# Performance work log

Hardware: AMD Instinct MI355X
Metric: run time of the kernel (lower is better)

## Reference

```python
import jax, jax.numpy as jnp
import numpy as np

B, F, M, N, H, O = 8, 128, 256, 1024, 64, 128
BN_EPS = 1e-5
COS_EPS = 1e-8


def _bn(x, g, b, m, v):
    # inference-mode BatchNorm over channel axis 1
    shape = [1] * x.ndim
    shape[1] = -1
    return g.reshape(shape) * (x - m.reshape(shape)) * jax.lax.rsqrt(v.reshape(shape) + BN_EPS) + b.reshape(shape)


def setup_inputs() -> dict:
    key = jax.random.key(0)
    ks = jax.random.split(key, 24)
    def n(k, shape, s=1.0):
        return jax.random.normal(k, shape, dtype=jnp.float32) * s
    inp = {}
    inp['template_feature'] = n(ks[0], (B, F, M))
    inp['search_feature'] = n(ks[1], (B, F, N))
    # SharedMLP 1x1 conv weights (bias=False because bn=True)
    inp['W1'] = n(ks[2], (H, F + 1), 0.05)
    inp['W2'] = n(ks[3], (H, H), 0.05)
    inp['W3'] = n(ks[4], (H, H), 0.05)
    # fea_layer: conv1d(H, bn=True) then conv1d(O, activation=None, bias=True)
    inp['Wc1'] = n(ks[5], (H, H), 0.05)
    inp['Wc2'] = n(ks[6], (O, H), 0.05)
    inp['bc2'] = n(ks[7], (O,), 0.05)
    for i, nm in enumerate(['1', '2', '3', 'c1']):
        inp['g' + nm] = 1.0 + n(ks[8 + i], (H,), 0.1)
        inp['b' + nm] = n(ks[12 + i], (H,), 0.1)
        inp['m' + nm] = n(ks[16 + i], (H,), 0.01)
        inp['v' + nm] = jax.random.uniform(ks[20 + i], (H,), minval=0.5, maxval=1.5, dtype=jnp.float32)
    return inp


def reference(template_feature, search_feature, W1, W2, W3, Wc1, Wc2, bc2,
              g1, b1, m1, v1, g2, b2, m2, v2, g3, b3, m3, v3, gc1, bc1, mc1, vc1):
    t, s = template_feature, search_feature
    # pairwise cosine similarity over channel dim (no BxFxMxN expand needed)
    dot = jnp.einsum('bfm,bfn->bmn', t, s)
    nt = jnp.linalg.norm(t, axis=1)  # (B, M)
    ns = jnp.linalg.norm(s, axis=1)  # (B, N)
    cos = dot / jnp.maximum(nt[:, :, None] * ns[:, None, :], COS_EPS)  # (B, M, N)
    # first 1x1 conv on concat(cos, expand(t)) computed fused (no concat materialization)
    h = jnp.einsum('hf,bfm->bhm', W1[:, 1:], t)[..., None] + W1[:, 0][None, :, None, None] * cos[:, None]
    h = jax.nn.relu(_bn(h, g1, b1, m1, v1))  # (B, H, M, N)
    h = jax.nn.relu(_bn(jnp.einsum('gh,bhmn->bgmn', W2, h), g2, b2, m2, v2))
    h = jax.nn.relu(_bn(jnp.einsum('gh,bhmn->bgmn', W3, h), g3, b3, m3, v3))
    p = jnp.max(h, axis=2)  # max-pool over M -> (B, H, N)
    c = jax.nn.relu(_bn(jnp.einsum('gh,bhn->bgn', Wc1, p), gc1, bc1, mc1, vc1))
    return jnp.einsum('oh,bhn->bon', Wc2, c) + bc2[None, :, None]  # (B, O, N)
```

## Files before the change

kernel.cpp:

```cpp
#include <hip/hip_runtime.h>


#define BB 8
#define FF 128
#define MM 256
#define NN 1024
#define HH 64
#define OO 128
#define BN_EPS 1e-5f
#define COS_EPS 1e-8f

#define WS_U     0
#define WS_C2    64
#define WS_C3    128
#define WS_CC1   192
#define WS_W2F   256
#define WS_W3F   4352
#define WS_WC1F  8448
#define WS_A1    12544
#define WS_NT    143616
#define WS_NS    145664
#define WS_COSH  153856
#define WS_P     1202432
#define PS       524288

typedef _Float16 half2v __attribute__((ext_vector_type(2)));
typedef _Float16 half8  __attribute__((ext_vector_type(8)));
typedef __attribute__((ext_vector_type(4))) float f32x4;

__device__ __forceinline__ unsigned int pkh2(float a, float b){
  auto h = __builtin_amdgcn_cvt_pkrtz(a, b);
  return __builtin_bit_cast(unsigned int, h);
}
__device__ __forceinline__ half2v u2h(unsigned int u){
  return __builtin_bit_cast(half2v, u);
}
__device__ __forceinline__ unsigned int h2u(half2v v){
  return __builtin_bit_cast(unsigned int, v);
}
__device__ __forceinline__ unsigned int relu2(unsigned int d){
  half2v v = __builtin_elementwise_max(u2h(d), (half2v){(_Float16)0, (_Float16)0});
  return h2u(v);
}
__device__ __forceinline__ unsigned int bh1(unsigned int up, half2v c, unsigned int ap){
  half2v v = __builtin_elementwise_fma(u2h(up), c, u2h(ap));
  v = __builtin_elementwise_max(v, (half2v){(_Float16)0, (_Float16)0});
  return h2u(v);
}
__device__ __forceinline__ float dot4(float4 a, float4 b, float acc){
  acc = fmaf(a.x, b.x, acc); acc = fmaf(a.y, b.y, acc);
  acc = fmaf(a.z, b.z, acc); acc = fmaf(a.w, b.w, acc);
  return acc;
}

__global__ __launch_bounds__(256) void k_prep(const float* t_, const float* s_,
    const float* W1, const float* W2, const float* W3, const float* Wc1,
    const float* g1, const float* b1, const float* m1, const float* v1,
    const float* g2, const float* b2, const float* m2, const float* v2,
    const float* g3, const float* b3, const float* m3, const float* v3,
    const float* gc1,const float* bc1,const float* mc1,const float* vc1,
    float* ws){
  __shared__ float W1s[64][133];
  int t = threadIdx.x;
  int bx = blockIdx.x;
  if (bx < 256){
    int b = bx >> 5, m0 = (bx & 31)*8;
    for (int idx = t; idx < 8192; idx += 256){
      int h = idx >> 7, f = idx & 127;
      W1s[h][f] = W1[h*129 + 1 + f];
    }
    __syncthreads();
    int h = t & 63, mg = t >> 6;
    const float* tp = t_ + (size_t)b*FF*MM + m0 + mg*2;
    float acc0 = 0.f, acc1 = 0.f;
    for (int f = 0; f < FF; f++){
      float wv = W1s[h][f];
      float2 tv = *(const float2*)&tp[(size_t)f*MM];
      acc0 = fmaf(wv, tv.x, acc0); acc1 = fmaf(wv, tv.y, acc1);
    }
    float a1 = g1[h] / sqrtf(v1[h] + BN_EPS);
    float c1 = b1[h] - a1*m1[h];
    unsigned short* dst = (unsigned short*)(ws + WS_A1) + ((size_t)(b*MM + m0 + mg*2))*64 + h;
    dst[0]  = (unsigned short)(pkh2(fmaf(a1, acc0, c1), 0.f) & 0xFFFFu);
    dst[64] = (unsigned short)(pkh2(fmaf(a1, acc1, c1), 0.f) & 0xFFFFu);
  } else if (bx < 416){
    __shared__ float red[4][64];
    int x = t & 63, fq = t >> 6;
    int idx = (bx - 256)*64 + x;
    const float* ptr; size_t stride;
    if (idx < BB*MM){
      int b = idx >> 8, m = idx & 255;
      ptr = t_ + (size_t)b*FF*MM + m; stride = MM;
    } else {
      int j = idx - BB*MM;
      int b = j >> 10, n = j & 1023;
      ptr = s_ + (size_t)b*FF*NN + n; stride = NN;
    }
    float acc = 0.f;
    for (int f = fq*32; f < fq*32 + 32; f++){
      float v = ptr[(size_t)f*stride]; acc = fmaf(v, v, acc);
    }
    red[fq][x] = acc;
    __syncthreads();
    if (fq == 0)
      ws[WS_NT + idx] = sqrtf(red[0][x] + red[1][x] + red[2][x] + red[3][x]);
  } else {
    if (t < 64){
      float a1 = g1[t] / sqrtf(v1[t] + BN_EPS);
      ws[WS_U + t]   = a1 * W1[t*129];
      float a2 = g2[t] / sqrtf(v2[t] + BN_EPS);
      ws[WS_C2 + t]  = b2[t] - a2*m2[t];
      float a3 = g3[t] / sqrtf(v3[t] + BN_EPS);
      ws[WS_C3 + t]  = b3[t] - a3*m3[t];
      float ac = gc1[t] / sqrtf(vc1[t] + BN_EPS);
      ws[WS_CC1 + t] = bc1[t] - ac*mc1[t];
    }
    for (int i = t; i < 4096; i += 256){
      int g = i >> 6;
      float a2 = g2[g] / sqrtf(v2[g] + BN_EPS);
      ws[WS_W2F + i]  = a2 * W2[i];
      float a3 = g3[g] / sqrtf(v3[g] + BN_EPS);
      ws[WS_W3F + i]  = a3 * W3[i];
      float ac = gc1[g] / sqrtf(vc1[g] + BN_EPS);
      ws[WS_WC1F + i] = ac * Wc1[i];
    }
  }
}

__global__ __launch_bounds__(256) void k_cos(const float* t_, const float* s_, float* ws){
  __shared__ __align__(16) unsigned short tS[64][136];
  __shared__ __align__(16) unsigned short sS[64][136];
  __shared__ float ntS[64], nsS[64];
  int t = threadIdx.x;
  int lane = t & 63, w = t >> 6;
  int ln15 = lane & 15, quad = lane >> 4;
  int m0 = blockIdx.x*64, n0 = blockIdx.y*64, b = blockIdx.z;
  {
    int x = t & 63;
    const float* tb = t_ + (size_t)b*FF*MM + m0 + x;
    const float* sb = s_ + (size_t)b*FF*NN + n0 + x;
    #pragma unroll
    for (int k = 0; k < 16; k++){
      int fp = w*16 + k;
      *(unsigned int*)&tS[x][2*fp] = pkh2(tb[(size_t)(2*fp)*MM], tb[(size_t)(2*fp+1)*MM]);
      *(unsigned int*)&sS[x][2*fp] = pkh2(sb[(size_t)(2*fp)*NN], sb[(size_t)(2*fp+1)*NN]);
    }
    if (t < 64) ntS[t] = ws[WS_NT + b*MM + m0 + t];
    else if (t < 128) nsS[t-64] = ws[WS_NS + b*NN + n0 + (t-64)];
  }
  __syncthreads();
  half8 A4[4];
  #pragma unroll
  for (int kc = 0; kc < 4; kc++)
    A4[kc] = *(const half8*)&tS[w*16 + ln15][kc*32 + quad*8];
  float4 nt4 = *(const float4*)&ntS[w*16 + quad*4];
  unsigned short* cosw = (unsigned short*)(ws + WS_COSH);
  #pragma unroll
  for (int ns = 0; ns < 4; ns++){
    f32x4 acc = (f32x4){0.f,0.f,0.f,0.f};
    #pragma unroll
    for (int kc = 0; kc < 4; kc++){
      half8 B4 = *(const half8*)&sS[ns*16 + ln15][kc*32 + quad*8];
      acc = __builtin_amdgcn_mfma_f32_16x16x32_f16(A4[kc], B4, acc, 0, 0, 0);
    }
    float nsv = nsS[ns*16 + ln15];
    int n = n0 + ns*16 + ln15;
    #pragma unroll
    for (int r = 0; r < 4; r++){
      int m = m0 + w*16 + quad*4 + r;
      float denom = fmaxf(nt4[r]*nsv, COS_EPS);
      float c = acc[r] * __builtin_amdgcn_rcpf(denom);
      cosw[(size_t)(b*MM + m)*NN + n] = (unsigned short)(pkh2(c, 0.f) & 0xFFFFu);
    }
  }
}

__global__ __launch_bounds__(256, 3) void k_main(const float* ws, float* Pp){
  __shared__ __align__(16) unsigned short h2W[4][16][72];
  int t = threadIdx.x;
  int lane = t & 63, w = t >> 6;
  int ln15 = lane & 15, quad = lane >> 4;
  int b = blockIdx.y;
  int n0 = blockIdx.x * 32;
  int ms = blockIdx.z;

  const float* w2p = ws + WS_W2F;
  const float* w3p = ws + WS_W3F;
  half8 W2A[4][2], W3A[4][2];
  f32x4 c2v[4], c3v[4];
  #pragma unroll
  for (int rt = 0; rt < 4; rt++){
    int g = rt*16 + ln15;
    #pragma unroll
    for (int kk = 0; kk < 2; kk++){
      half8 a2, a3;
      #pragma unroll
      for (int j = 0; j < 8; j++){
        int k = kk*32 + quad*8 + j;
        a2[j] = (_Float16)w2p[g*64 + k];
        a3[j] = (_Float16)w3p[g*64 + k];
      }
      W2A[rt][kk] = a2; W3A[rt][kk] = a3;
    }
    float4 cb2 = *(const float4*)&ws[WS_C2 + rt*16 + quad*4];
    float4 cb3 = *(const float4*)&ws[WS_C3 + rt*16 + quad*4];
    c2v[rt] = (f32x4){cb2.x, cb2.y, cb2.z, cb2.w};
    c3v[rt] = (f32x4){cb3.x, cb3.y, cb3.z, cb3.w};
  }
  unsigned int upk[2][4];
  #pragma unroll
  for (int kk = 0; kk < 2; kk++){
    float4 ua = *(const float4*)&ws[WS_U + kk*32 + quad*8];
    float4 ub = *(const float4*)&ws[WS_U + kk*32 + quad*8 + 4];
    upk[kk][0] = pkh2(ua.x, ua.y); upk[kk][1] = pkh2(ua.z, ua.w);
    upk[kk][2] = pkh2(ub.x, ub.y); upk[kk][3] = pkh2(ub.z, ub.w);
  }
  const unsigned short* A1H = (const unsigned short*)(ws + WS_A1) + (size_t)b*MM*64;
  int mp = w >> 1;
  int n  = n0 + (w & 1)*16 + ln15;
  const unsigned short* cosP = (const unsigned short*)(ws + WS_COSH)
                               + (size_t)b*MM*NN + n;
  unsigned short* h2w = &h2W[w][0][0];

  f32x4 p[4];
  #pragma unroll
  for (int rt = 0; rt < 4; rt++) p[rt] = (f32x4){0.f,0.f,0.f,0.f};

  int m0i = ms*128 + mp;
  unsigned int cu = cosP[(size_t)m0i*NN];
  uint4 a1a = *(const uint4*)&A1H[(size_t)m0i*64 + quad*8];
  uint4 a1b = *(const uint4*)&A1H[(size_t)m0i*64 + 32 + quad*8];

  for (int mc = 0; mc < 64; mc++){
    int mN = ms*128 + (mc < 63 ? (mc + 1) : 63)*2 + mp;
    unsigned int cuN = cosP[(size_t)mN*NN];
    uint4 a1aN = *(const uint4*)&A1H[(size_t)mN*64 + quad*8];
    uint4 a1bN = *(const uint4*)&A1H[(size_t)mN*64 + 32 + quad*8];

    unsigned int cd = cu | (cu << 16);
    half2v ch = u2h(cd);
    uint4 q0, q1;
    q0.x = bh1(upk[0][0], ch, a1a.x); q0.y = bh1(upk[0][1], ch, a1a.y);
    q0.z = bh1(upk[0][2], ch, a1a.z); q0.w = bh1(upk[0][3], ch, a1a.w);
    q1.x = bh1(upk[1][0], ch, a1b.x); q1.y = bh1(upk[1][1], ch, a1b.y);
    q1.z = bh1(upk[1][2], ch, a1b.z); q1.w = bh1(upk[1][3], ch, a1b.w);
    half8 b0h = __builtin_bit_cast(half8, q0);
    half8 b1h = __builtin_bit_cast(half8, q1);

    f32x4 acc[4];
    #pragma unroll
    for (int rt = 0; rt < 4; rt++){
      acc[rt] = __builtin_amdgcn_mfma_f32_16x16x32_f16(W2A[rt][0], b0h, c2v[rt], 0, 0, 0);
      acc[rt] = __builtin_amdgcn_mfma_f32_16x16x32_f16(W2A[rt][1], b1h, acc[rt], 0, 0, 0);
    }
    #pragma unroll
    for (int rt = 0; rt < 4; rt++){
      uint2 vv;
      vv.x = relu2(pkh2(acc[rt][0], acc[rt][1]));
      vv.y = relu2(pkh2(acc[rt][2], acc[rt][3]));
      *(uint2*)&h2w[ln15*72 + rt*16 + quad*4] = vv;
    }
    __asm__ volatile("s_waitcnt lgkmcnt(0)" ::: "memory");
    half8 e0 = *(const half8*)&h2w[ln15*72 + quad*8];
    half8 e1 = *(const half8*)&h2w[ln15*72 + 32 + quad*8];
    #pragma unroll
    for (int rt = 0; rt < 4; rt++){
      f32x4 a3 = __builtin_amdgcn_mfma_f32_16x16x32_f16(W3A[rt][0], e0, c3v[rt], 0, 0, 0);
      a3 = __builtin_amdgcn_mfma_f32_16x16x32_f16(W3A[rt][1], e1, a3, 0, 0, 0);
      #pragma unroll
      for (int r = 0; r < 4; r++) p[rt][r] = fmaxf(p[rt][r], a3[r]);
    }
    cu = cuN; a1a = a1aN; a1b = a1bN;
  }

  __syncthreads();
  float* redBuf = (float*)&h2W[0][0][0];
  if (w >= 2){
    #pragma unroll
    for (int rt = 0; rt < 4; rt++){
      f32x4 v = p[rt];
      *(float4*)&redBuf[(size_t)(((w & 1)*16 + ln15)*66 + rt*16 + quad*4)] =
          make_float4(v[0], v[1], v[2], v[3]);
    }
  }
  __syncthreads();
  if (w < 2){
    float* Pb = Pp + (size_t)ms*PS + ((size_t)(b*NN + n) << 6);
    #pragma unroll
    for (int rt = 0; rt < 4; rt++){
      float4 o = *(const float4*)&redBuf[(size_t)(((w & 1)*16 + ln15)*66 + rt*16 + quad*4)];
      float4 r4;
      r4.x = fmaxf(p[rt][0], o.x);
      r4.y = fmaxf(p[rt][1], o.y);
      r4.z = fmaxf(p[rt][2], o.z);
      r4.w = fmaxf(p[rt][3], o.w);
      *(float4*)&Pb[rt*16 + quad*4] = r4;
    }
  }
}

__global__ __launch_bounds__(256) void k_tail(const float* Wc2, const float* bc2,
                                              const float* ws, float* out){
  __shared__ float WT[64][68];
  __shared__ float pT[32][68];
  __shared__ float cS[32][68];
  int t = threadIdx.x;
  int n0 = blockIdx.x * 32;
  int b = blockIdx.y;
  for (int i = t; i < 4096; i += 256) WT[i >> 6][i & 63] = ws[WS_WC1F + i];
  const float* P0 = ws + WS_P + ((size_t)(b*NN + n0) << 6);
  const float* P1 = P0 + PS;
  for (int i = t; i < 2048; i += 256) pT[i >> 6][i & 63] = fmaxf(P0[i], P1[i]);
  __syncthreads();
  {
    int n = t & 31, q = t >> 5;
    for (int k = 0; k < 8; k++){
      int g = q*8 + k;
      float acc = ws[WS_CC1 + g];
      for (int hs = 0; hs < 64; hs += 4){
        float4 wv = *(const float4*)&WT[g][hs];
        float4 pv = *(const float4*)&pT[n][hs];
        acc = dot4(wv, pv, acc);
      }
      cS[n][g] = fmaxf(acc, 0.f);
    }
  }
  __syncthreads();
  {
    int o = t & 127, hf = t >> 7;
    float bco = bc2[o];
    float accO[16];
    #pragma unroll
    for (int i = 0; i < 16; i++) accO[i] = bco;
    for (int hs = 0; hs < 64; hs += 4){
      float4 w4 = *(const float4*)&Wc2[o*64 + hs];
      #pragma unroll
      for (int i = 0; i < 16; i++){
        float4 cv = *(const float4*)&cS[hf*16 + i][hs];
        accO[i] = dot4(w4, cv, accO[i]);
      }
    }
    #pragma unroll
    for (int i = 0; i < 16; i++)
      out[((size_t)(b*OO + o))*NN + n0 + hf*16 + i] = accO[i];
  }
}

extern "C" void kernel_launch(void* const* d_in, const int* in_sizes, int n_in,
                              void* d_out, int out_size, void* d_ws, size_t ws_size,
                              hipStream_t stream){
  (void)in_sizes; (void)n_in; (void)out_size; (void)ws_size;
  const float* t_  = (const float*)d_in[0];
  const float* s_  = (const float*)d_in[1];
  const float* W1  = (const float*)d_in[2];
  const float* W2  = (const float*)d_in[3];
  const float* W3  = (const float*)d_in[4];
  const float* Wc1 = (const float*)d_in[5];
  const float* Wc2 = (const float*)d_in[6];
  const float* bc2 = (const float*)d_in[7];
  const float* g1 = (const float*)d_in[8],  *b1 = (const float*)d_in[9],
             * m1 = (const float*)d_in[10], *v1 = (const float*)d_in[11];
  const float* g2 = (const float*)d_in[12], *b2 = (const float*)d_in[13],
             * m2 = (const float*)d_in[14], *v2 = (const float*)d_in[15];
  const float* g3 = (const float*)d_in[16], *b3 = (const float*)d_in[17],
             * m3 = (const float*)d_in[18], *v3 = (const float*)d_in[19];
  const float* gc1 = (const float*)d_in[20], *bc1 = (const float*)d_in[21],
             * mc1 = (const float*)d_in[22], *vc1 = (const float*)d_in[23];
  float* ws = (float*)d_ws;
  float* out = (float*)d_out;

  k_prep<<<417, 256, 0, stream>>>(t_, s_, W1, W2, W3, Wc1,
      g1,b1,m1,v1, g2,b2,m2,v2, g3,b3,m3,v3, gc1,bc1,mc1,vc1, ws);
  k_cos<<<dim3(4, 16, 8), 256, 0, stream>>>(t_, s_, ws);
  k_main<<<dim3(32, 8, 2), 256, 0, stream>>>(ws, ws + WS_P);
  k_tail<<<dim3(32, 8), 256, 0, stream>>>(Wc2, bc2, ws, out);
}
```

Baseline: 187.7 us.

## Split k_main over more blocks with 16-wide n tiles and fp16 prepacked weights

k_main now gives each block 16 n columns instead of 32, so the grid doubles to 1024 blocks. All four waves now split the M range four ways instead of two, and a three-slot shared buffer does the cross-wave max reduction. The W2/W3 folded weights are now stored as fp16 in the prep kernel, so each thread loads half8 vectors directly instead of converting 16 scalar floats. The launch bound is raised to 4 blocks per SM. The aim is better occupancy and GPU fill for the main loop, at the cost of more redundant weight loads per block and register pressure under the tighter bound.

```diff
diff --git a/kernel.cpp b/kernel.cpp
--- a/kernel.cpp
+++ b/kernel.cpp
@@ -14,8 +14,8 @@
 #define WS_C2    64
 #define WS_C3    128
 #define WS_CC1   192
-#define WS_W2F   256
-#define WS_W3F   4352
+#define WS_W2H   256
+#define WS_W3H   2304
 #define WS_WC1F  8448
 #define WS_A1    12544
 #define WS_NT    143616
@@ -115,12 +115,14 @@
       float ac = gc1[t] / sqrtf(vc1[t] + BN_EPS);
       ws[WS_CC1 + t] = bc1[t] - ac*mc1[t];
     }
+    unsigned short* w2h = (unsigned short*)(ws + WS_W2H);
+    unsigned short* w3h = (unsigned short*)(ws + WS_W3H);
     for (int i = t; i < 4096; i += 256){
       int g = i >> 6;
       float a2 = g2[g] / sqrtf(v2[g] + BN_EPS);
-      ws[WS_W2F + i]  = a2 * W2[i];
+      w2h[i] = __builtin_bit_cast(unsigned short, (_Float16)(a2 * W2[i]));
       float a3 = g3[g] / sqrtf(v3[g] + BN_EPS);
-      ws[WS_W3F + i]  = a3 * W3[i];
+      w3h[i] = __builtin_bit_cast(unsigned short, (_Float16)(a3 * W3[i]));
       float ac = gc1[g] / sqrtf(vc1[g] + BN_EPS);
       ws[WS_WC1F + i] = ac * Wc1[i];
     }
@@ -175,17 +177,18 @@
   }
 }
 
-__global__ __launch_bounds__(256, 3) void k_main(const float* ws, float* Pp){
+__global__ __launch_bounds__(256, 4) void k_main(const float* ws, float* Pp){
   __shared__ __align__(16) unsigned short h2W[4][16][72];
+  __shared__ __align__(16) float redS[3][16][68];
   int t = threadIdx.x;
   int lane = t & 63, w = t >> 6;
   int ln15 = lane & 15, quad = lane >> 4;
   int b = blockIdx.y;
-  int n0 = blockIdx.x * 32;
+  int n0 = blockIdx.x * 16;
   int ms = blockIdx.z;
 
-  const float* w2p = ws + WS_W2F;
-  const float* w3p = ws + WS_W3F;
+  const unsigned short* w2h = (const unsigned short*)(ws + WS_W2H);
+  const unsigned short* w3h = (const unsigned short*)(ws + WS_W3H);
   half8 W2A[4][2], W3A[4][2];
   f32x4 c2v[4], c3v[4];
   #pragma unroll
@@ -193,14 +196,8 @@
     int g = rt*16 + ln15;
     #pragma unroll
     for (int kk = 0; kk < 2; kk++){
-      half8 a2, a3;
-      #pragma unroll
-      for (int j = 0; j < 8; j++){
-        int k = kk*32 + quad*8 + j;
-        a2[j] = (_Float16)w2p[g*64 + k];
-        a3[j] = (_Float16)w3p[g*64 + k];
-      }
-      W2A[rt][kk] = a2; W3A[rt][kk] = a3;
+      W2A[rt][kk] = *(const half8*)&w2h[g*64 + kk*32 + quad*8];
+      W3A[rt][kk] = *(const half8*)&w3h[g*64 + kk*32 + quad*8];
     }
     float4 cb2 = *(const float4*)&ws[WS_C2 + rt*16 + quad*4];
     float4 cb3 = *(const float4*)&ws[WS_C3 + rt*16 + quad*4];
@@ -216,8 +213,7 @@
     upk[kk][2] = pkh2(ub.x, ub.y); upk[kk][3] = pkh2(ub.z, ub.w);
   }
   const unsigned short* A1H = (const unsigned short*)(ws + WS_A1) + (size_t)b*MM*64;
-  int mp = w >> 1;
-  int n  = n0 + (w & 1)*16 + ln15;
+  int n = n0 + ln15;
   const unsigned short* cosP = (const unsigned short*)(ws + WS_COSH)
                                + (size_t)b*MM*NN + n;
   unsigned short* h2w = &h2W[w][0][0];
@@ -226,13 +222,13 @@
   #pragma unroll
   for (int rt = 0; rt < 4; rt++) p[rt] = (f32x4){0.f,0.f,0.f,0.f};
 
-  int m0i = ms*128 + mp;
+  int m0i = ms*128 + w;
   unsigned int cu = cosP[(size_t)m0i*NN];
   uint4 a1a = *(const uint4*)&A1H[(size_t)m0i*64 + quad*8];
   uint4 a1b = *(const uint4*)&A1H[(size_t)m0i*64 + 32 + quad*8];
 
-  for (int mc = 0; mc < 64; mc++){
-    int mN = ms*128 + (mc < 63 ? (mc + 1) : 63)*2 + mp;
+  for (int mc = 0; mc < 32; mc++){
+    int mN = ms*128 + (mc < 31 ? (mc + 1) : 31)*4 + w;
     unsigned int cuN = cosP[(size_t)mN*NN];
     uint4 a1aN = *(const uint4*)&A1H[(size_t)mN*64 + quad*8];
     uint4 a1bN = *(const uint4*)&A1H[(size_t)mN*64 + 32 + quad*8];
@@ -274,26 +270,26 @@
   }
 
   __syncthreads();
-  float* redBuf = (float*)&h2W[0][0][0];
-  if (w >= 2){
+  if (w >= 1){
     #pragma unroll
     for (int rt = 0; rt < 4; rt++){
       f32x4 v = p[rt];
-      *(float4*)&redBuf[(size_t)(((w & 1)*16 + ln15)*66 + rt*16 + quad*4)] =
-          make_float4(v[0], v[1], v[2], v[3]);
-    }
-  }
-  __syncthreads();
-  if (w < 2){
+      *(float4*)&redS[w-1][ln15][rt*16 + quad*4] = make_float4(v[0], v[1], v[2], v[3]);
+    }
+  }
+  __syncthreads();
+  if (w == 0){
     float* Pb = Pp + (size_t)ms*PS + ((size_t)(b*NN + n) << 6);
     #pragma unroll
     for (int rt = 0; rt < 4; rt++){
-      float4 o = *(const float4*)&redBuf[(size_t)(((w & 1)*16 + ln15)*66 + rt*16 + quad*4)];
+      float4 o1 = *(const float4*)&redS[0][ln15][rt*16 + quad*4];
+      float4 o2 = *(const float4*)&redS[1][ln15][rt*16 + quad*4];
+      float4 o3 = *(const float4*)&redS[2][ln15][rt*16 + quad*4];
       float4 r4;
-      r4.x = fmaxf(p[rt][0], o.x);
-      r4.y = fmaxf(p[rt][1], o.y);
-      r4.z = fmaxf(p[rt][2], o.z);
-      r4.w = fmaxf(p[rt][3], o.w);
+      r4.x = fmaxf(fmaxf(p[rt][0], o1.x), fmaxf(o2.x, o3.x));
+      r4.y = fmaxf(fmaxf(p[rt][1], o1.y), fmaxf(o2.y, o3.y));
+      r4.z = fmaxf(fmaxf(p[rt][2], o1.z), fmaxf(o2.z, o3.z));
+      r4.w = fmaxf(fmaxf(p[rt][3], o1.w), fmaxf(o2.w, o3.w));
       *(float4*)&Pb[rt*16 + quad*4] = r4;
     }
   }
@@ -372,6 +368,6 @@
   k_prep<<<417, 256, 0, stream>>>(t_, s_, W1, W2, W3, Wc1,
       g1,b1,m1,v1, g2,b2,m2,v2, g3,b3,m3,v3, gc1,bc1,mc1,vc1, ws);
   k_cos<<<dim3(4, 16, 8), 256, 0, stream>>>(t_, s_, ws);
-  k_main<<<dim3(32, 8, 2), 256, 0, stream>>>(ws, ws + WS_P);
+  k_main<<<dim3(64, 8, 2), 256, 0, stream>>>(ws, ws + WS_P);
   k_tail<<<dim3(32, 8), 256, 0, stream>>>(Wc2, bc2, ws, out);
 }
```

Result: slower. 267.1 us (+42.3%).
